# Performance work log

Hardware: AMD Instinct MI355X
Metric: run time of the kernel (lower is better)

Reference implementation:

```python
import jax, jax.numpy as jnp
import numpy as np

B, F, R, O = 32768, 64, 64, 64  # batch, in_features, rules, out_features


def setup_inputs() -> dict:
    key = jax.random.key(0)
    k1, k2, k3, k4, k5 = jax.random.split(key, 5)
    X = jax.random.normal(k1, (B, F), dtype=jnp.float32)
    tt = jax.random.normal(k2, (1, F, R), dtype=jnp.float32) * 0.01
    mean = jax.random.normal(k3, (1, F, R), dtype=jnp.float32)
    # std is a learned positive scale (set by _rule_initialization); keep it away from 0
    std = jax.random.uniform(k4, (1, F, R), dtype=jnp.float32, minval=0.5, maxval=1.5)
    W = jax.random.normal(k5, (O, R * (F + 1)), dtype=jnp.float32) * 0.02  # nn.Linear weight [out, in]
    return {"X": X, "tt": tt, "mean": mean, "std": std, "W": W}


def reference(X, tt, mean, std, W):
    t = jnp.tanh(tt)                                  # [1,F,R]
    z = (X[:, :, None] - mean) / std                  # [B,F,R]
    g = jnp.exp(-(z * z))                             # Gaussian membership [B,F,R]
    m = g * t + 0.5 * (1.0 - t)                       # affine blend toward 0.5
    fire = jnp.prod(m, axis=1)                        # product t-norm over features -> [B,R]
    w = fire / jnp.sum(fire, axis=1, keepdims=True)   # normalize over rules
    ones = jnp.ones((X.shape[0], 1), dtype=X.dtype)
    Xa = jnp.concatenate([X, ones], axis=1)           # [B,F+1]
    feat = (Xa[:, :, None] * w[:, None, :]).reshape(X.shape[0], -1)  # [B,(F+1)*R], row-major (f outer, r inner)
    return feat @ W.T                                 # [B,O]
```

## Files before the change

### kernel.cpp

```cpp
#include <hip/hip_runtime.h>
#include <hip/hip_bf16.h>

#define F 64
#define R 64
#define O 64
#define BLOCK_B 64

typedef short bf16x8 __attribute__((ext_vector_type(8)));
typedef float f32x4 __attribute__((ext_vector_type(4)));
typedef float f32x2 __attribute__((ext_vector_type(2)));

static __device__ __forceinline__ short f2bf(float f) {
    unsigned u = __builtin_bit_cast(unsigned, f);
    unsigned r = (u + 0x7fffu + ((u >> 16) & 1u)) >> 16;
    return (short)r;
}

__global__ __launch_bounds__(256) void fq_prep(
        const float* __restrict__ tt, const float* __restrict__ mean,
        const float* __restrict__ std_, const float* __restrict__ W,
        float* __restrict__ prm, unsigned short* __restrict__ Wpk)
{
    const int blk = blockIdx.x;
    const int t   = threadIdx.x;
    if (blk < 65) {
        const int f = blk;
        __shared__ __align__(16) float ws[64][68];
#pragma unroll
        for (int i = 0; i < 16; ++i) {
            const int o = i * 4 + (t >> 6);
            const int r = t & 63;
            ws[o][r] = W[(size_t)o * 4160 + f * 64 + r];
        }
        __syncthreads();
#pragma unroll
        for (int half = 0; half < 2; ++half) {
            const int u8   = half * 256 + t;
            const int lane = u8 & 63;
            const int kk   = (u8 >> 6) & 1;
            const int nt   = u8 >> 7;
            const int o    = nt * 16 + (lane & 15);
            const int rb   = ((lane >> 4) << 3) + kk * 32;
            f32x4 a = *(const f32x4*)&ws[o][rb];
            f32x4 b = *(const f32x4*)&ws[o][rb + 4];
            unsigned short v[8];
            v[0] = (unsigned short)f2bf(a[0]); v[1] = (unsigned short)f2bf(a[1]);
            v[2] = (unsigned short)f2bf(a[2]); v[3] = (unsigned short)f2bf(a[3]);
            v[4] = (unsigned short)f2bf(b[0]); v[5] = (unsigned short)f2bf(b[1]);
            v[6] = (unsigned short)f2bf(b[2]); v[7] = (unsigned short)f2bf(b[3]);
            const int dst = ((nt * 65 + f) * 2 + kk) * 64 + lane;
            *(bf16x8*)(Wpk + (size_t)dst * 8) = *(bf16x8*)v;
        }
    } else {
#pragma unroll
        for (int i = 0; i < 16; ++i) {
            const int u = i * 256 + t;
            float sd = std_[u];
            float mn = mean[u];
            float th = tanhf(tt[u]);
            float s  = 1.2011224087864498f / sd;
            float4 p;
            p.x = s;
            p.y = mn * s;
            p.z = th;
            p.w = 0.5f * (1.0f - th);
            ((float4*)prm)[u] = p;
        }
    }
}

__global__ __launch_bounds__(1024, 8) void fq_main(
        const float* __restrict__ X,
        const float4* __restrict__ prm,
        const bf16x8* __restrict__ Wp,
        float* __restrict__ out)
{
    __shared__ __align__(16) float xt[64][68];
    __shared__ __align__(16) float fire_lds[64][68];
    __shared__ float rinv[BLOCK_B];

    const int t    = threadIdx.x;
    const int lane = t & 63;
    const int w    = __builtin_amdgcn_readfirstlane(t >> 6);
    const int b0   = blockIdx.x * BLOCK_B;

    {
        const int row = t & 63;
        const int f4  = (t >> 6) * 4;
        float4 xv = *(const float4*)(X + (size_t)(b0 + row) * 64 + f4);
        xt[f4 + 0][row] = xv.x;
        xt[f4 + 1][row] = xv.y;
        xt[f4 + 2][row] = xv.z;
        xt[f4 + 3][row] = xv.w;
    }
    __syncthreads();

    {
        f32x2 fire2[2] = {(f32x2){1.f, 1.f}, (f32x2){1.f, 1.f}};
        const int r0 = 4 * w;
#pragma unroll 4
        for (int f = 0; f < F; ++f) {
            float4 p = prm[f * 64 + lane];
            f32x2 x01 = *(const f32x2*)&xt[f][r0];
            f32x2 x23 = *(const f32x2*)&xt[f][r0 + 2];
            f32x2 z0, z1;
            z0.x = __builtin_fmaf(x01.x, p.x, -p.y);
            z0.y = __builtin_fmaf(x01.y, p.x, -p.y);
            z1.x = __builtin_fmaf(x23.x, p.x, -p.y);
            z1.y = __builtin_fmaf(x23.y, p.x, -p.y);
            f32x2 nz0 = -(z0 * z0), nz1 = -(z1 * z1);
            f32x2 g0, g1;
            g0.x = __builtin_amdgcn_exp2f(nz0.x);
            g0.y = __builtin_amdgcn_exp2f(nz0.y);
            g1.x = __builtin_amdgcn_exp2f(nz1.x);
            g1.y = __builtin_amdgcn_exp2f(nz1.y);
            f32x2 t2 = (f32x2){p.z, p.z};
            f32x2 c2 = (f32x2){p.w, p.w};
            fire2[0] *= g0 * t2 + c2;
            fire2[1] *= g1 * t2 + c2;
        }
        fire_lds[r0 + 0][lane] = fire2[0].x;
        fire_lds[r0 + 1][lane] = fire2[0].y;
        fire_lds[r0 + 2][lane] = fire2[1].x;
        fire_lds[r0 + 3][lane] = fire2[1].y;
    }
    __syncthreads();

    if (t < 512) {
        const int row = t >> 3;
        const int c8  = (t & 7) * 8;
        f32x4 s0 = *(const f32x4*)&fire_lds[row][c8];
        f32x4 s1 = *(const f32x4*)&fire_lds[row][c8 + 4];
        float s = (s0[0] + s0[1]) + (s0[2] + s0[3]) +
                  (s1[0] + s1[1]) + (s1[2] + s1[3]);
        s += __shfl_xor(s, 1);
        s += __shfl_xor(s, 2);
        s += __shfl_xor(s, 4);
        if ((t & 7) == 0) rinv[row] = 1.0f / s;
    }
    __syncthreads();

    const int m_in  = lane & 15;
    const int quad  = lane >> 4;
    const int nt    = w >> 2;
    const int mrow  = w & 3;
    const int myrow = 16 * mrow + m_in;
    const float rs  = rinv[myrow];
    const int q8    = quad * 8;

    bf16x8 wfrag[2];
#pragma unroll
    for (int kk = 0; kk < 2; ++kk)
#pragma unroll
        for (int j = 0; j < 8; ++j)
            wfrag[kk][j] = f2bf(fire_lds[myrow][q8 + j + kk * 32] * rs);

    const bf16x8* wpb = Wp + (size_t)(nt * 130) * 64 + lane;
    const int xoff = 16 * mrow + quad * 4;

    f32x4 acc = (f32x4){0.f, 0.f, 0.f, 0.f};
    const f32x4 z4 = (f32x4){0.f, 0.f, 0.f, 0.f};

#pragma unroll 4
    for (int f = 0; f < F; ++f) {
        bf16x8 bb0 = wpb[(2 * f) * 64];
        bf16x8 bb1 = wpb[(2 * f + 1) * 64];
        f32x4 U = __builtin_amdgcn_mfma_f32_16x16x32_bf16(wfrag[0], bb0, z4, 0, 0, 0);
        U = __builtin_amdgcn_mfma_f32_16x16x32_bf16(wfrag[1], bb1, U, 0, 0, 0);
        f32x4 xv = *(const f32x4*)&xt[f][xoff];
#pragma unroll
        for (int reg = 0; reg < 4; ++reg)
            acc[reg] = __builtin_fmaf(xv[reg], U[reg], acc[reg]);
    }

    {
        bf16x8 bb0 = wpb[128 * 64];
        bf16x8 bb1 = wpb[129 * 64];
        f32x4 U = __builtin_amdgcn_mfma_f32_16x16x32_bf16(wfrag[0], bb0, z4, 0, 0, 0);
        U = __builtin_amdgcn_mfma_f32_16x16x32_bf16(wfrag[1], bb1, U, 0, 0, 0);
#pragma unroll
        for (int reg = 0; reg < 4; ++reg)
            acc[reg] += U[reg];
    }

#pragma unroll
    for (int reg = 0; reg < 4; ++reg) {
        const int row = b0 + 16 * mrow + quad * 4 + reg;
        out[(size_t)row * 64 + nt * 16 + m_in] = acc[reg];
    }
}

extern "C" void kernel_launch(void* const* d_in, const int* in_sizes, int n_in,
                              void* d_out, int out_size, void* d_ws, size_t ws_size,
                              hipStream_t stream) {
    const float* X    = (const float*)d_in[0];
    const float* tt   = (const float*)d_in[1];
    const float* mean = (const float*)d_in[2];
    const float* std_ = (const float*)d_in[3];
    const float* W    = (const float*)d_in[4];
    float* out = (float*)d_out;

    float* prm = (float*)d_ws;
    unsigned short* Wpk = (unsigned short*)((char*)d_ws + 65536);

    fq_prep<<<66, 256, 0, stream>>>(tt, mean, std_, W, prm, Wpk);

    const int nblocks = 32768 / BLOCK_B;
    fq_main<<<nblocks, 1024, 0, stream>>>(X, (const float4*)prm,
                                          (const bf16x8*)Wpk, out);
}
```

Baseline: 120.3 us.

## Shrink blocks to 256 threads and reuse W fragments across four M tiles

The main kernel now runs 256-thread blocks of four waves. In the membership phase each wave computes 16 batch rows, reading X directly from global memory with wave-uniform addresses instead of through the LDS transpose. In the GEMM phase each wave owns one 16-column output tile and loops over all four 16-row M tiles, so each loaded W fragment feeds four MFMA pairs instead of one. This cuts W fragment traffic and barrier cost, but it raises per-thread register pressure (8 fire accumulators, 8 A fragments, 4 accumulators) and leaves fewer waves per block to hide exp and memory latency.

```diff
diff --git a/kernel.cpp b/kernel.cpp
--- a/kernel.cpp
+++ b/kernel.cpp
@@ -69,7 +69,7 @@
     }
 }
 
-__global__ __launch_bounds__(1024, 8) void fq_main(
+__global__ __launch_bounds__(256, 2) void fq_main(
         const float* __restrict__ X,
         const float4* __restrict__ prm,
         const bf16x8* __restrict__ Wp,
@@ -85,109 +85,131 @@
     const int b0   = blockIdx.x * BLOCK_B;
 
     {
-        const int row = t & 63;
-        const int f4  = (t >> 6) * 4;
-        float4 xv = *(const float4*)(X + (size_t)(b0 + row) * 64 + f4);
-        xt[f4 + 0][row] = xv.x;
-        xt[f4 + 1][row] = xv.y;
-        xt[f4 + 2][row] = xv.z;
-        xt[f4 + 3][row] = xv.w;
-    }
-    __syncthreads();
-
-    {
-        f32x2 fire2[2] = {(f32x2){1.f, 1.f}, (f32x2){1.f, 1.f}};
-        const int r0 = 4 * w;
-#pragma unroll 4
+        const int f4 = (t & 15) * 4;
+        const int r0 = t >> 4;
+#pragma unroll
+        for (int it = 0; it < 4; ++it) {
+            const int row = r0 + 16 * it;
+            float4 xv = *(const float4*)(X + (size_t)(b0 + row) * 64 + f4);
+            xt[f4 + 0][row] = xv.x;
+            xt[f4 + 1][row] = xv.y;
+            xt[f4 + 2][row] = xv.z;
+            xt[f4 + 3][row] = xv.w;
+        }
+    }
+
+    {
+        f32x2 fire2[8];
+#pragma unroll
+        for (int i = 0; i < 8; ++i) fire2[i] = (f32x2){1.f, 1.f};
+        const float* Xw = X + (size_t)(b0 + 16 * w) * 64;
+#pragma unroll 2
         for (int f = 0; f < F; ++f) {
             float4 p = prm[f * 64 + lane];
-            f32x2 x01 = *(const f32x2*)&xt[f][r0];
-            f32x2 x23 = *(const f32x2*)&xt[f][r0 + 2];
-            f32x2 z0, z1;
-            z0.x = __builtin_fmaf(x01.x, p.x, -p.y);
-            z0.y = __builtin_fmaf(x01.y, p.x, -p.y);
-            z1.x = __builtin_fmaf(x23.x, p.x, -p.y);
-            z1.y = __builtin_fmaf(x23.y, p.x, -p.y);
-            f32x2 nz0 = -(z0 * z0), nz1 = -(z1 * z1);
-            f32x2 g0, g1;
-            g0.x = __builtin_amdgcn_exp2f(nz0.x);
-            g0.y = __builtin_amdgcn_exp2f(nz0.y);
-            g1.x = __builtin_amdgcn_exp2f(nz1.x);
-            g1.y = __builtin_amdgcn_exp2f(nz1.y);
             f32x2 t2 = (f32x2){p.z, p.z};
             f32x2 c2 = (f32x2){p.w, p.w};
-            fire2[0] *= g0 * t2 + c2;
-            fire2[1] *= g1 * t2 + c2;
-        }
-        fire_lds[r0 + 0][lane] = fire2[0].x;
-        fire_lds[r0 + 1][lane] = fire2[0].y;
-        fire_lds[r0 + 2][lane] = fire2[1].x;
-        fire_lds[r0 + 3][lane] = fire2[1].y;
+#pragma unroll
+            for (int i = 0; i < 8; ++i) {
+                float x0 = Xw[(2 * i) * 64 + f];
+                float x1 = Xw[(2 * i + 1) * 64 + f];
+                f32x2 z;
+                z.x = __builtin_fmaf(x0, p.x, -p.y);
+                z.y = __builtin_fmaf(x1, p.x, -p.y);
+                f32x2 nz = -(z * z);
+                f32x2 g;
+                g.x = __builtin_amdgcn_exp2f(nz.x);
+                g.y = __builtin_amdgcn_exp2f(nz.y);
+                fire2[i] *= g * t2 + c2;
+            }
+        }
+#pragma unroll
+        for (int i = 0; i < 8; ++i) {
+            fire_lds[16 * w + 2 * i][lane]     = fire2[i].x;
+            fire_lds[16 * w + 2 * i + 1][lane] = fire2[i].y;
+        }
     }
     __syncthreads();
 
-    if (t < 512) {
-        const int row = t >> 3;
-        const int c8  = (t & 7) * 8;
-        f32x4 s0 = *(const f32x4*)&fire_lds[row][c8];
-        f32x4 s1 = *(const f32x4*)&fire_lds[row][c8 + 4];
-        float s = (s0[0] + s0[1]) + (s0[2] + s0[3]) +
-                  (s1[0] + s1[1]) + (s1[2] + s1[3]);
+    {
+        const int row = t >> 2;
+        const int c16 = (t & 3) * 16;
+        f32x4 s0 = *(const f32x4*)&fire_lds[row][c16];
+        f32x4 s1 = *(const f32x4*)&fire_lds[row][c16 + 4];
+        f32x4 s2 = *(const f32x4*)&fire_lds[row][c16 + 8];
+        f32x4 s3 = *(const f32x4*)&fire_lds[row][c16 + 12];
+        float s = ((s0[0] + s0[1]) + (s0[2] + s0[3])) +
+                  ((s1[0] + s1[1]) + (s1[2] + s1[3])) +
+                  ((s2[0] + s2[1]) + (s2[2] + s2[3])) +
+                  ((s3[0] + s3[1]) + (s3[2] + s3[3]));
         s += __shfl_xor(s, 1);
         s += __shfl_xor(s, 2);
-        s += __shfl_xor(s, 4);
-        if ((t & 7) == 0) rinv[row] = 1.0f / s;
+        if ((t & 3) == 0) rinv[row] = 1.0f / s;
     }
     __syncthreads();
 
-    const int m_in  = lane & 15;
-    const int quad  = lane >> 4;
-    const int nt    = w >> 2;
-    const int mrow  = w & 3;
-    const int myrow = 16 * mrow + m_in;
-    const float rs  = rinv[myrow];
-    const int q8    = quad * 8;
-
-    bf16x8 wfrag[2];
-#pragma unroll
-    for (int kk = 0; kk < 2; ++kk)
-#pragma unroll
-        for (int j = 0; j < 8; ++j)
-            wfrag[kk][j] = f2bf(fire_lds[myrow][q8 + j + kk * 32] * rs);
+    const int m_in = lane & 15;
+    const int quad = lane >> 4;
+    const int nt   = w;
+    const int q8   = quad * 8;
+
+    bf16x8 wfrag[4][2];
+#pragma unroll
+    for (int m = 0; m < 4; ++m) {
+        const int myrow = 16 * m + m_in;
+        const float rs  = rinv[myrow];
+#pragma unroll
+        for (int kk = 0; kk < 2; ++kk) {
+            f32x4 a = *(const f32x4*)&fire_lds[myrow][q8 + kk * 32];
+            f32x4 b = *(const f32x4*)&fire_lds[myrow][q8 + kk * 32 + 4];
+            wfrag[m][kk][0] = f2bf(a[0] * rs); wfrag[m][kk][1] = f2bf(a[1] * rs);
+            wfrag[m][kk][2] = f2bf(a[2] * rs); wfrag[m][kk][3] = f2bf(a[3] * rs);
+            wfrag[m][kk][4] = f2bf(b[0] * rs); wfrag[m][kk][5] = f2bf(b[1] * rs);
+            wfrag[m][kk][6] = f2bf(b[2] * rs); wfrag[m][kk][7] = f2bf(b[3] * rs);
+        }
+    }
 
     const bf16x8* wpb = Wp + (size_t)(nt * 130) * 64 + lane;
-    const int xoff = 16 * mrow + quad * 4;
-
-    f32x4 acc = (f32x4){0.f, 0.f, 0.f, 0.f};
+
+    f32x4 acc[4];
+#pragma unroll
+    for (int m = 0; m < 4; ++m) acc[m] = (f32x4){0.f, 0.f, 0.f, 0.f};
     const f32x4 z4 = (f32x4){0.f, 0.f, 0.f, 0.f};
 
 #pragma unroll 4
     for (int f = 0; f < F; ++f) {
         bf16x8 bb0 = wpb[(2 * f) * 64];
         bf16x8 bb1 = wpb[(2 * f + 1) * 64];
-        f32x4 U = __builtin_amdgcn_mfma_f32_16x16x32_bf16(wfrag[0], bb0, z4, 0, 0, 0);
-        U = __builtin_amdgcn_mfma_f32_16x16x32_bf16(wfrag[1], bb1, U, 0, 0, 0);
-        f32x4 xv = *(const f32x4*)&xt[f][xoff];
-#pragma unroll
-        for (int reg = 0; reg < 4; ++reg)
-            acc[reg] = __builtin_fmaf(xv[reg], U[reg], acc[reg]);
+#pragma unroll
+        for (int m = 0; m < 4; ++m) {
+            f32x4 U = __builtin_amdgcn_mfma_f32_16x16x32_bf16(wfrag[m][0], bb0, z4, 0, 0, 0);
+            U = __builtin_amdgcn_mfma_f32_16x16x32_bf16(wfrag[m][1], bb1, U, 0, 0, 0);
+            f32x4 xv = *(const f32x4*)&xt[f][16 * m + quad * 4];
+#pragma unroll
+            for (int reg = 0; reg < 4; ++reg)
+                acc[m][reg] = __builtin_fmaf(xv[reg], U[reg], acc[m][reg]);
+        }
     }
 
     {
         bf16x8 bb0 = wpb[128 * 64];
         bf16x8 bb1 = wpb[129 * 64];
-        f32x4 U = __builtin_amdgcn_mfma_f32_16x16x32_bf16(wfrag[0], bb0, z4, 0, 0, 0);
-        U = __builtin_amdgcn_mfma_f32_16x16x32_bf16(wfrag[1], bb1, U, 0, 0, 0);
-#pragma unroll
-        for (int reg = 0; reg < 4; ++reg)
-            acc[reg] += U[reg];
-    }
-
-#pragma unroll
-    for (int reg = 0; reg < 4; ++reg) {
-        const int row = b0 + 16 * mrow + quad * 4 + reg;
-        out[(size_t)row * 64 + nt * 16 + m_in] = acc[reg];
-    }
+#pragma unroll
+        for (int m = 0; m < 4; ++m) {
+            f32x4 U = __builtin_amdgcn_mfma_f32_16x16x32_bf16(wfrag[m][0], bb0, z4, 0, 0, 0);
+            U = __builtin_amdgcn_mfma_f32_16x16x32_bf16(wfrag[m][1], bb1, U, 0, 0, 0);
+#pragma unroll
+            for (int reg = 0; reg < 4; ++reg)
+                acc[m][reg] += U[reg];
+        }
+    }
+
+#pragma unroll
+    for (int m = 0; m < 4; ++m)
+#pragma unroll
+        for (int reg = 0; reg < 4; ++reg) {
+            const int row = b0 + 16 * m + quad * 4 + reg;
+            out[(size_t)row * 64 + nt * 16 + m_in] = acc[m][reg];
+        }
 }
 
 extern "C" void kernel_launch(void* const* d_in, const int* in_sizes, int n_in,
@@ -206,6 +228,6 @@
     fq_prep<<<66, 256, 0, stream>>>(tt, mean, std_, W, prm, Wpk);
 
     const int nblocks = 32768 / BLOCK_B;
-    fq_main<<<nblocks, 1024, 0, stream>>>(X, (const float4*)prm,
-                                          (const bf16x8*)Wpk, out);
-}
+    fq_main<<<nblocks, 256, 0, stream>>>(X, (const float4*)prm,
+                                         (const bf16x8*)Wpk, out);
+}
```

Result: faster. 117.4 us (-2.4%).
